# Kernel tuning notes

Measured on AMD Instinct MI355X. Metric: run time of the kernel, lower is better.

## Reference

```python
import jax, jax.numpy as jnp
import numpy as np

LRELU_SLOPE = 0.2
LN_EPS = 1e-5
BAND_EPS = 1e-8


def setup_inputs() -> dict:
    key = jax.random.key(0)
    ks = jax.random.split(key, 3)
    B, C, H, W = 32, 3, 1024, 1024
    num_bands, feat_dim = 16, 256
    fin = C * num_bands * 3  # 144
    x = jax.random.normal(ks[0], (B, C, H, W), dtype=jnp.float32)
    W1 = jax.random.normal(ks[1], (fin, feat_dim), dtype=jnp.float32) * 0.05
    b1 = jnp.zeros((feat_dim,), jnp.float32)
    W2 = jax.random.normal(ks[2], (feat_dim, feat_dim), dtype=jnp.float32) * 0.05
    b2 = jnp.zeros((feat_dim,), jnp.float32)
    gamma = jnp.ones((feat_dim,), jnp.float32)
    beta = jnp.zeros((feat_dim,), jnp.float32)
    return {"x": x, "W1": W1, "b1": b1, "W2": W2, "b2": b2, "gamma": gamma, "beta": beta}


def reference(x, W1, b1, W2, b2, gamma, beta):
    B, C, H, W = x.shape
    nb = W1.shape[0] // (C * 3)  # num_bands
    # --- FFT magnitude ---
    mag = jnp.abs(jnp.fft.rfft2(x, norm='ortho'))  # [B,C,H,Wr]
    Wr = mag.shape[-1]
    # --- radial bin index (exact same >= comparisons as the torch band loop) ---
    u = jnp.fft.rfftfreq(W).astype(mag.dtype)          # [Wr]
    v = jnp.fft.fftfreq(H).astype(mag.dtype)           # [H]
    radius = jnp.sqrt(u[None, :] ** 2 + v[:, None] ** 2)  # [H,Wr]
    max_r = radius.max()
    lowers = max_r * jnp.arange(nb + 1, dtype=mag.dtype) / nb  # i=0..nb
    # bin = (#thresholds <= radius) - 1 ; radius==max_r lands in segment nb (excluded)
    bins = jnp.sum(radius[..., None] >= lowers[None, None, :], axis=-1) - 1  # [H,Wr]
    seg = bins.reshape(-1).astype(jnp.int32)  # [H*Wr]
    K = nb + 1
    # --- single-pass segmented reductions over all pixels ---
    magf = mag.reshape(B * C, -1).T                      # [HWr, B*C]
    counts = jax.ops.segment_sum(jnp.ones(seg.shape, mag.dtype), seg, num_segments=K)  # [K]
    s1 = jax.ops.segment_sum(magf, seg, num_segments=K)             # [K, BC]
    s2 = jax.ops.segment_sum(magf * magf, seg, num_segments=K)      # [K, BC]
    mx = jax.ops.segment_max(magf, seg, num_segments=K)             # [K, BC]
    denom = counts[:, None] + BAND_EPS
    mean = s1 / denom
    # sum over band of (mag-mean)^2 = s2 - 2*mean*s1 + count*mean^2
    var = (s2 - 2.0 * mean * s1 + counts[:, None] * mean * mean) / denom
    # drop segment nb (radius == max_r is excluded by `radius < upper`), then sqrt
    mean = mean[:nb]
    var = jnp.maximum(var[:nb], 0.0)
    std = jnp.sqrt(var)
    # torch max is over mag*mask (zeros elsewhere) -> floor at 0
    mx = jnp.maximum(mx[:nb], 0.0)
    # --- assemble [B, nb*3*C] in band-major, (mean,max,std), channel order ---
    def to_bkc(a):
        return a.reshape(nb, B, C).transpose(1, 0, 2)  # [B, nb, C]
    feat_vec = jnp.stack([to_bkc(mean), to_bkc(mx), to_bkc(std)], axis=2)  # [B, nb, 3, C]
    feat_vec = feat_vec.reshape(B, nb * 3 * C)
    # --- MLP: Linear -> LeakyReLU(0.2) -> Linear -> LayerNorm ---
    h = feat_vec @ W1 + b1
    h = jnp.where(h >= 0, h, LRELU_SLOPE * h)
    h = h @ W2 + b2
    mu = jnp.mean(h, axis=-1, keepdims=True)
    va = jnp.mean((h - mu) ** 2, axis=-1, keepdims=True)
    return (h - mu) / jnp.sqrt(va + LN_EPS) * gamma + beta
```

## Files before the change

kernel.cpp:

```cpp
#include <hip/hip_runtime.h>
#include <hip/hip_fp16.h>
#include <math.h>

#define HH    1024
#define WWID  1024
#define WR    513
#define NIMG  96
#define NGRP  65
#define KSEG  17
#define FEAT  256
#define FIN   144

__device__ __forceinline__ float2 cmul(float2 a, float2 b) {
    return make_float2(a.x * b.x - a.y * b.y, a.x * b.y + a.y * b.x);
}

__device__ __forceinline__ int radial_bin(int hf, int k) {
    const float maxr = 0.707106781186547524f;
    float v = (float)(hf < 512 ? hf : hf - 1024) * (1.0f / 1024.0f);
    float u = (float)k * (1.0f / 1024.0f);
    float rad = sqrtf(u * u + v * v);
    int bin = 0;
#pragma unroll
    for (int l = 1; l <= 16; ++l) {
        float lower = (maxr * (float)l) * 0.0625f;
        bin += (rad >= lower) ? 1 : 0;
    }
    return bin;
}

__device__ __forceinline__ int fast_bin(float rad) {
    int c = (int)(rad * 22.62741699796952f);
    if (c > 16) c = 16;
    if (c < 16 && rad >= (0.707106781186547524f * (float)(c + 1)) * 0.0625f) c++;
    else if (rad < (0.707106781186547524f * (float)c) * 0.0625f) c--;
    return c;
}

__device__ __forceinline__ float2 wave_fft_AB(float2 a[16], int l) {
    constexpr float TW16C[8] = {1.f, 0.9238795325112867f, 0.7071067811865476f,
                                0.3826834323650898f, 0.f, -0.3826834323650898f,
                                -0.7071067811865476f, -0.9238795325112867f};
    constexpr float TW16S[8] = {0.f, -0.3826834323650898f, -0.7071067811865476f,
                                -0.9238795325112867f, -1.f, -0.9238795325112867f,
                                -0.7071067811865476f, -0.3826834323650898f};
#pragma unroll
    for (int m = 2; m <= 16; m <<= 1) {
        const int half = m >> 1;
        const int tstep = 16 / m;
#pragma unroll
        for (int bse = 0; bse < 16; bse += m) {
#pragma unroll
            for (int jj = 0; jj < 8; ++jj) {
                if (jj < half) {
                    float2 w = make_float2(TW16C[jj * tstep], TW16S[jj * tstep]);
                    float2 tv = cmul(a[bse + half + jj], w);
                    float2 u0 = a[bse + jj];
                    a[bse + jj]        = make_float2(u0.x + tv.x, u0.y + tv.y);
                    a[bse + half + jj] = make_float2(u0.x - tv.x, u0.y - tv.y);
                }
            }
        }
    }
    float ang = (float)l * (-6.28318530717958647692f / 1024.0f);
    float2 w1 = make_float2(__cosf(ang), __sinf(ang));
    float2 w2 = cmul(w1, w1);
    float2 w3 = cmul(w2, w1);
    float2 w4 = cmul(w2, w2);
    float2 w8 = cmul(w4, w4);
    float2 w12 = cmul(w8, w4);
    a[1] = cmul(a[1], w1);
    a[2] = cmul(a[2], w2);
    a[3] = cmul(a[3], w3);
#pragma unroll
    for (int r = 4; r < 16; ++r) {
        float2 hi = (r >> 2) == 1 ? w4 : ((r >> 2) == 2 ? w8 : w12);
        float2 p = cmul(a[r], hi);
        int lo = r & 3;
        if (lo == 1) p = cmul(p, w1);
        else if (lo == 2) p = cmul(p, w2);
        else if (lo == 3) p = cmul(p, w3);
        a[r] = p;
    }
    return cmul(w8, w8);
}

__device__ __forceinline__ void wave_fft_C(float2 a[16], int l, float2 u) {
#pragma unroll
    for (int half = 32; half >= 1; half >>= 1) {
        const bool up = (l & half) != 0;
        const float sgn = up ? -1.0f : 1.0f;
        const float twx = up ? -u.x : 1.0f;
        const float twy = up ? -u.y : 0.0f;
#pragma unroll
        for (int r = 0; r < 16; ++r) {
            float ox = __shfl_xor(a[r].x, half);
            float oy = __shfl_xor(a[r].y, half);
            float sx = fmaf(sgn, a[r].x, ox);
            float sy = fmaf(sgn, a[r].y, oy);
            a[r].x = fmaf(sx, twx, -(sy * twy));
            a[r].y = fmaf(sx, twy, sy * twx);
        }
        if (half > 1) u = cmul(u, u);
    }
}

static __device__ __constant__ int BR4[16] = {0,8,4,12,2,10,6,14,1,9,5,13,3,11,7,15};

__global__ __launch_bounds__(1024) void k_rowfft(const float* __restrict__ x,
                                                 __half2* __restrict__ interm,
                                                 int img0) {
    __shared__ __half2 tile[1024][17];
    const int t = threadIdx.x;
    const int w = t >> 6;
    const int l = t & 63;
    const int blk = blockIdx.x;
    const int iy = blockIdx.y;
    const int img = img0 + iy;
    const int hA = ((w & 7) << 6) + 2 * blk + (w >> 3);
    const int hB = hA + 512;

    const float* r1 = x + ((size_t)img * HH + hA) * WWID;
    const float* r2 = x + ((size_t)img * HH + hB) * WWID;
    float2 a[16];
#pragma unroll
    for (int j = 0; j < 16; ++j) {
        int i = l + 64 * j;
        a[BR4[j]] = make_float2(r1[i], r2[i]);
    }

    float2 u16 = wave_fft_AB(a, l);
    wave_fft_C(a, l, u16);

    const int b = (int)(__brev((unsigned)l) >> 26);
#pragma unroll
    for (int r = 0; r < 16; ++r) {
        int k = 16 * b + r;
        tile[k][w ^ (b & 15)] = __floats2half2_rn(a[r].x, a[r].y);
    }
    __syncthreads();

    __half2* gout = interm + (size_t)iy * 1024 * 512 + blk * 16;
#pragma unroll
    for (int it = 0; it < 16; ++it) {
        int idx = t + it * 1024;
        int k = idx >> 4;
        int s = idx & 15;
        gout[(size_t)k * 512 + s] = tile[k][s ^ ((k >> 4) & 15)];
    }
}

__global__ __launch_bounds__(512) void k_colfft(const __half2* __restrict__ interm,
                                                float* __restrict__ partials,
                                                int img0) {
    __shared__ float wsum[8][KSEG][2];
    __shared__ unsigned wmax[8][KSEG];
    const int t = threadIdx.x;
    const int g = blockIdx.x;
    const int iy = blockIdx.y;
    const int img = img0 + iy;
    const int wv = t >> 6;
    const int l = t & 63;
    const int k = g * 8 + wv;

    for (int i = t; i < 8 * KSEG; i += 512) {
        int w = i / KSEG, bb = i - w * KSEG;
        wsum[w][bb][0] = 0.f; wsum[w][bb][1] = 0.f; wmax[w][bb] = 0u;
    }
    __syncthreads();

    if (k <= 512) {
        const int kn = (1024 - k) & 1023;
        const uint4* ps = (const uint4*)(interm + ((size_t)iy * 1024 + k) * 512 + l * 8);
        const uint4* pn = (const uint4*)(interm + ((size_t)iy * 1024 + kn) * 512 + l * 8);
        union QU { uint4 q[2]; __half2 h[8]; } us, un;
        us.q[0] = ps[0]; us.q[1] = ps[1];
        un.q[0] = pn[0]; un.q[1] = pn[1];

        float2 a[16];
#pragma unroll
        for (int m = 0; m < 8; ++m) {
            float2 zs = __half22float2(us.h[m]);
            float2 zn = __half22float2(un.h[m]);
            a[BR4[m]]     = make_float2(0.5f * (zs.x + zn.x), 0.5f * (zs.y - zn.y));
            a[BR4[m + 8]] = make_float2(0.5f * (zs.y + zn.y), 0.5f * (zn.x - zs.x));
        }

        float2 u16 = wave_fft_AB(a, l);
        wave_fft_C(a, l, u16);

        const int b = (int)(__brev((unsigned)l) >> 26);
        const int h0 = 16 * b;
        const float uf = (float)k * (1.0f / 1024.0f);
        const float uu = uf * uf;
        float vf0 = (float)(h0 < 512 ? h0 : h0 - 1024) * (1.0f / 1024.0f);
        float vfF = (float)(h0 + 15 < 512 ? h0 + 15 : h0 + 15 - 1024) * (1.0f / 1024.0f);
        int binF = fast_bin(sqrtf(fmaf(vf0, vf0, uu)));
        int binL = fast_bin(sqrtf(fmaf(vfF, vfF, uu)));
        const int bHi = (binF > binL) ? binF : binL;
        const float Lmid = (0.707106781186547524f * (float)bHi) * 0.0625f;
        const float Lmid2 = Lmid * Lmid;

        float sA1 = 0.f, sA2 = 0.f, mA = 0.f;
        float sB1 = 0.f, sB2 = 0.f, mB = 0.f;
#pragma unroll
        for (int r = 0; r < 16; ++r) {
            int h = h0 + r;
            float vf = (float)(h < 512 ? h : h - 1024) * (1.0f / 1024.0f);
            float s = fmaf(vf, vf, uu);
            float2 z = a[r];
            float p2 = fmaf(z.x, z.x, z.y * z.y);
            float m = sqrtf(p2) * (1.0f / 1024.0f);
            float msq = p2 * (1.0f / 1048576.0f);
            bool c = (s >= Lmid2);
            sA1 += c ? m : 0.f;
            sA2 += c ? msq : 0.f;
            mA = fmaxf(mA, c ? m : 0.f);
            sB1 += c ? 0.f : m;
            sB2 += c ? 0.f : msq;
            mB = fmaxf(mB, c ? 0.f : m);
        }

        atomicAdd(&wsum[wv][bHi][0], sA1);
        atomicAdd(&wsum[wv][bHi][1], sA2);
        atomicMax(&wmax[wv][bHi], __float_as_uint(mA));
        if (bHi > 0) {
            atomicAdd(&wsum[wv][bHi - 1][0], sB1);
            atomicAdd(&wsum[wv][bHi - 1][1], sB2);
            atomicMax(&wmax[wv][bHi - 1], __float_as_uint(mB));
        }
    }
    __syncthreads();

    if (t < KSEG) {
        float aS = 0.f, bS = 0.f, cM = 0.f;
#pragma unroll
        for (int w = 0; w < 8; ++w) {
            aS += wsum[w][t][0];
            bS += wsum[w][t][1];
            cM = fmaxf(cM, __uint_as_float(wmax[w][t]));
        }
        float* dstp = partials + ((size_t)img * NGRP + g) * (KSEG * 3) + t * 3;
        dstp[0] = aS; dstp[1] = bS; dstp[2] = cM;
    }
}

__global__ __launch_bounds__(256) void k_counts(unsigned* __restrict__ counts) {
    int cnt[KSEG];
#pragma unroll
    for (int l = 0; l < KSEG; ++l) cnt[l] = 0;
    const int total = HH * WR;
    for (int idx = blockIdx.x * 256 + threadIdx.x; idx < total; idx += gridDim.x * 256) {
        int h = idx / WR;
        int k = idx - h * WR;
        int bin = radial_bin(h, k);
#pragma unroll
        for (int l = 0; l < KSEG; ++l) cnt[l] += (bin == l) ? 1 : 0;
    }
    const int lane = threadIdx.x & 63;
#pragma unroll
    for (int l = 0; l < KSEG; ++l) {
        int c = cnt[l];
        for (int off = 32; off > 0; off >>= 1) c += __shfl_xor(c, off);
        if (lane == 0 && c > 0) atomicAdd(&counts[l], (unsigned)c);
    }
}

__global__ __launch_bounds__(256) void k_mlp(const float* __restrict__ partials,
                                             const unsigned* __restrict__ counts,
                                             const float* __restrict__ W1,
                                             const float* __restrict__ b1,
                                             const float* __restrict__ W2,
                                             const float* __restrict__ b2,
                                             const float* __restrict__ gamma,
                                             const float* __restrict__ beta,
                                             float* __restrict__ out) {
    __shared__ float feat[FIN];
    __shared__ float h1s[FEAT];
    __shared__ float red[FEAT];
    const int b = blockIdx.x;
    const int t = threadIdx.x;
    if (t < 48) {
        int c = t / 16;
        int bin = t % 16;
        const float* p = partials + ((size_t)(b * 3 + c) * NGRP) * (KSEG * 3) + bin * 3;
        float s1 = 0.f, s2 = 0.f, mxv = 0.f;
        for (int gg = 0; gg < NGRP; ++gg) {
            s1 += p[gg * (KSEG * 3) + 0];
            s2 += p[gg * (KSEG * 3) + 1];
            mxv = fmaxf(mxv, p[gg * (KSEG * 3) + 2]);
        }
        float cntf = (float)counts[bin];
        float denom = cntf + 1e-8f;
        float mean = s1 / denom;
        float var = (s2 - 2.0f * mean * s1 + cntf * mean * mean) / denom;
        var = fmaxf(var, 0.0f);
        float sd = sqrtf(var);
        mxv = fmaxf(mxv, 0.0f);
        feat[bin * 9 + 0 + c] = mean;
        feat[bin * 9 + 3 + c] = mxv;
        feat[bin * 9 + 6 + c] = sd;
    }
    __syncthreads();

    float acc = b1[t];
    for (int i = 0; i < FIN; ++i) acc += feat[i] * W1[i * FEAT + t];
    acc = (acc >= 0.0f) ? acc : 0.2f * acc;
    h1s[t] = acc;
    __syncthreads();

    float acc2 = b2[t];
    for (int i = 0; i < FEAT; ++i) acc2 += h1s[i] * W2[i * FEAT + t];

    red[t] = acc2;
    __syncthreads();
    for (int off = 128; off > 0; off >>= 1) {
        if (t < off) red[t] += red[t + off];
        __syncthreads();
    }
    float mu = red[0] * (1.0f / 256.0f);
    __syncthreads();
    float dvt = acc2 - mu;
    red[t] = dvt * dvt;
    __syncthreads();
    for (int off = 128; off > 0; off >>= 1) {
        if (t < off) red[t] += red[t + off];
        __syncthreads();
    }
    float va = red[0] * (1.0f / 256.0f);
    out[(size_t)b * FEAT + t] = dvt / sqrtf(va + 1e-5f) * gamma[t] + beta[t];
}

extern "C" void kernel_launch(void* const* d_in, const int* in_sizes, int n_in,
                              void* d_out, int out_size, void* d_ws, size_t ws_size,
                              hipStream_t stream) {
    const float* x     = (const float*)d_in[0];
    const float* W1    = (const float*)d_in[1];
    const float* b1    = (const float*)d_in[2];
    const float* W2    = (const float*)d_in[3];
    const float* b2    = (const float*)d_in[4];
    const float* gamma = (const float*)d_in[5];
    const float* beta  = (const float*)d_in[6];
    float* out = (float*)d_out;

    char* ws = (char*)d_ws;
    unsigned* counts = (unsigned*)ws;
    float* partials = (float*)(ws + 256);
    const size_t partialsBytes = (size_t)NIMG * NGRP * KSEG * 3 * sizeof(float);
    const size_t intermOff = (256 + partialsBytes + 255) & ~(size_t)255;
    __half2* interm = (__half2*)(ws + intermOff);
    const size_t perImg = (size_t)1024 * 512 * sizeof(__half2);

    long long avail = (long long)ws_size - (long long)intermOff;
    int chunk = (avail > 0) ? (int)(avail / (long long)perImg) : 0;
    if (chunk > NIMG) chunk = NIMG;
    if (chunk < 1) chunk = 1;

    hipMemsetAsync(counts, 0, KSEG * sizeof(unsigned), stream);
    k_counts<<<dim3(128), dim3(256), 0, stream>>>(counts);

    for (int img0 = 0; img0 < NIMG; img0 += chunk) {
        int n = NIMG - img0;
        if (n > chunk) n = chunk;
        k_rowfft<<<dim3(32, n), dim3(1024), 0, stream>>>(x, interm, img0);
        k_colfft<<<dim3(NGRP, n), dim3(512), 0, stream>>>(interm, partials, img0);
    }

    k_mlp<<<dim3(32), dim3(256), 0, stream>>>(partials, counts, W1, b1, W2, b2,
                                              gamma, beta, out);
}
```

Before: 447.0 us.

## Restructure row FFT for vectorized loads, swizzle shuffles, and slotted LDS atomics

The row FFT now loads each row with contiguous float4 reads and reverses the decomposition order: the cross-lane stages run first, then twiddles, then the in-register radix-16. This lets each lane hold contiguous input elements. Cross-lane shuffles use ds_swizzle for lane distances below 32 and ds_bpermute for 32, replacing generic shfl_xor. In the column kernel, the shared-memory atomic accumulators are spread over 8 slots per wave to cut contention, and the 1/1024 scaling is moved out of the inner loop. The risks are a larger shared-memory footprint, a duplicated init loop, and the removed XOR swizzle on the row tile, which may bring back LDS bank conflicts.

```diff
diff --git a/kernel.cpp b/kernel.cpp
--- a/kernel.cpp
+++ b/kernel.cpp
@@ -37,7 +37,45 @@
     return c;
 }
 
-__device__ __forceinline__ float2 wave_fft_AB(float2 a[16], int l) {
+__device__ constexpr int BR4[16] = {0,8,4,12,2,10,6,14,1,9,5,13,3,11,7,15};
+
+template<int HALF>
+__device__ __forceinline__ float sxl(float v, int addr32) {
+    if constexpr (HALF == 32)
+        return __int_as_float(__builtin_amdgcn_ds_bpermute(addr32, __float_as_int(v)));
+    else
+        return __int_as_float(__builtin_amdgcn_ds_swizzle(__float_as_int(v),
+                                                          (HALF << 10) | 0x1F));
+}
+
+template<int HALF>
+__device__ __forceinline__ void fftC_stage(float2 a[16], int l, float2 u, int addr32) {
+    const bool up = (l & HALF) != 0;
+    const float sgn = up ? -1.0f : 1.0f;
+    const float twx = up ? -u.x : 1.0f;
+    const float twy = up ? -u.y : 0.0f;
+#pragma unroll
+    for (int r = 0; r < 16; ++r) {
+        float ox = sxl<HALF>(a[r].x, addr32);
+        float oy = sxl<HALF>(a[r].y, addr32);
+        float sx = fmaf(sgn, a[r].x, ox);
+        float sy = fmaf(sgn, a[r].y, oy);
+        a[r].x = fmaf(sx, twx, -(sy * twy));
+        a[r].y = fmaf(sx, twy, sy * twx);
+    }
+}
+
+__device__ __forceinline__ void wave_fft_C(float2 a[16], int l, float2 u) {
+    const int addr32 = ((l ^ 32) << 2);
+    fftC_stage<32>(a, l, u, addr32); u = cmul(u, u);
+    fftC_stage<16>(a, l, u, addr32); u = cmul(u, u);
+    fftC_stage<8>(a, l, u, addr32);  u = cmul(u, u);
+    fftC_stage<4>(a, l, u, addr32);  u = cmul(u, u);
+    fftC_stage<2>(a, l, u, addr32);  u = cmul(u, u);
+    fftC_stage<1>(a, l, u, addr32);
+}
+
+__device__ __forceinline__ void fft16_regs(float2 a[16]) {
     constexpr float TW16C[8] = {1.f, 0.9238795325112867f, 0.7071067811865476f,
                                 0.3826834323650898f, 0.f, -0.3826834323650898f,
                                 -0.7071067811865476f, -0.9238795325112867f};
@@ -62,50 +100,31 @@
             }
         }
     }
-    float ang = (float)l * (-6.28318530717958647692f / 1024.0f);
+}
+
+template<bool PERM>
+__device__ __forceinline__ void twiddle_regs(float2 a[16], float ang, float2* w16out) {
     float2 w1 = make_float2(__cosf(ang), __sinf(ang));
     float2 w2 = cmul(w1, w1);
     float2 w3 = cmul(w2, w1);
     float2 w4 = cmul(w2, w2);
     float2 w8 = cmul(w4, w4);
     float2 w12 = cmul(w8, w4);
-    a[1] = cmul(a[1], w1);
-    a[2] = cmul(a[2], w2);
-    a[3] = cmul(a[3], w3);
-#pragma unroll
-    for (int r = 4; r < 16; ++r) {
-        float2 hi = (r >> 2) == 1 ? w4 : ((r >> 2) == 2 ? w8 : w12);
-        float2 p = cmul(a[r], hi);
-        int lo = r & 3;
+#pragma unroll
+    for (int r = 1; r < 16; ++r) {
+        const int e = PERM ? BR4[r] : r;
+        float2 p = a[r];
+        const int hi = e >> 2, lo = e & 3;
+        if (hi == 1) p = cmul(p, w4);
+        else if (hi == 2) p = cmul(p, w8);
+        else if (hi == 3) p = cmul(p, w12);
         if (lo == 1) p = cmul(p, w1);
         else if (lo == 2) p = cmul(p, w2);
         else if (lo == 3) p = cmul(p, w3);
         a[r] = p;
     }
-    return cmul(w8, w8);
-}
-
-__device__ __forceinline__ void wave_fft_C(float2 a[16], int l, float2 u) {
-#pragma unroll
-    for (int half = 32; half >= 1; half >>= 1) {
-        const bool up = (l & half) != 0;
-        const float sgn = up ? -1.0f : 1.0f;
-        const float twx = up ? -u.x : 1.0f;
-        const float twy = up ? -u.y : 0.0f;
-#pragma unroll
-        for (int r = 0; r < 16; ++r) {
-            float ox = __shfl_xor(a[r].x, half);
-            float oy = __shfl_xor(a[r].y, half);
-            float sx = fmaf(sgn, a[r].x, ox);
-            float sy = fmaf(sgn, a[r].y, oy);
-            a[r].x = fmaf(sx, twx, -(sy * twy));
-            a[r].y = fmaf(sx, twy, sy * twx);
-        }
-        if (half > 1) u = cmul(u, u);
-    }
-}
-
-static __device__ __constant__ int BR4[16] = {0,8,4,12,2,10,6,14,1,9,5,13,3,11,7,15};
+    if (w16out) *w16out = cmul(w8, w8);
+}
 
 __global__ __launch_bounds__(1024) void k_rowfft(const float* __restrict__ x,
                                                  __half2* __restrict__ interm,
@@ -120,24 +139,33 @@
     const int hA = ((w & 7) << 6) + 2 * blk + (w >> 3);
     const int hB = hA + 512;
 
-    const float* r1 = x + ((size_t)img * HH + hA) * WWID;
-    const float* r2 = x + ((size_t)img * HH + hB) * WWID;
+    const float4* r1 = (const float4*)(x + ((size_t)img * HH + hA) * WWID) + 4 * l;
+    const float4* r2 = (const float4*)(x + ((size_t)img * HH + hB) * WWID) + 4 * l;
+    float4 f1[4], f2[4];
+#pragma unroll
+    for (int c = 0; c < 4; ++c) { f1[c] = r1[c]; f2[c] = r2[c]; }
+
     float2 a[16];
 #pragma unroll
     for (int j = 0; j < 16; ++j) {
-        int i = l + 64 * j;
-        a[BR4[j]] = make_float2(r1[i], r2[i]);
-    }
-
-    float2 u16 = wave_fft_AB(a, l);
-    wave_fft_C(a, l, u16);
+        float v1 = ((const float*)f1)[j];
+        float v2 = ((const float*)f2)[j];
+        a[BR4[j]] = make_float2(v1, v2);
+    }
+
+    float angL = (float)l * (-6.28318530717958647692f / 64.0f);
+    wave_fft_C(a, l, make_float2(__cosf(angL), __sinf(angL)));
 
     const int b = (int)(__brev((unsigned)l) >> 26);
-#pragma unroll
-    for (int r = 0; r < 16; ++r) {
-        int k = 16 * b + r;
-        tile[k][w ^ (b & 15)] = __floats2half2_rn(a[r].x, a[r].y);
-    }
+
+    float angB = (float)b * (-6.28318530717958647692f / 1024.0f);
+    twiddle_regs<true>(a, angB, nullptr);
+
+    fft16_regs(a);
+
+#pragma unroll
+    for (int r = 0; r < 16; ++r)
+        tile[b + 64 * r][w] = __floats2half2_rn(a[r].x, a[r].y);
     __syncthreads();
 
     __half2* gout = interm + (size_t)iy * 1024 * 512 + blk * 16;
@@ -146,15 +174,15 @@
         int idx = t + it * 1024;
         int k = idx >> 4;
         int s = idx & 15;
-        gout[(size_t)k * 512 + s] = tile[k][s ^ ((k >> 4) & 15)];
+        gout[(size_t)k * 512 + s] = tile[k][s];
     }
 }
 
 __global__ __launch_bounds__(512) void k_colfft(const __half2* __restrict__ interm,
                                                 float* __restrict__ partials,
                                                 int img0) {
-    __shared__ float wsum[8][KSEG][2];
-    __shared__ unsigned wmax[8][KSEG];
+    __shared__ float wsum[8][KSEG][8][2];
+    __shared__ unsigned wmax[8][KSEG][8];
     const int t = threadIdx.x;
     const int g = blockIdx.x;
     const int iy = blockIdx.y;
@@ -162,10 +190,25 @@
     const int wv = t >> 6;
     const int l = t & 63;
     const int k = g * 8 + wv;
-
-    for (int i = t; i < 8 * KSEG; i += 512) {
-        int w = i / KSEG, bb = i - w * KSEG;
-        wsum[w][bb][0] = 0.f; wsum[w][bb][1] = 0.f; wmax[w][bb] = 0u;
+    const int slot = l & 7;
+
+    for (int i = t; i < 8 * KSEG * 8; i += 512) {
+        int w = i >> 7;
+        int rem = i - w * 136;
+        if (w < 8 && rem < 136) {
+            int bb = rem >> 3, sl = rem & 7;
+            wsum[w][bb][sl][0] = 0.f;
+            wsum[w][bb][sl][1] = 0.f;
+            wmax[w][bb][sl] = 0u;
+        }
+    }
+    for (int i = t; i < 8 * 136; i += 512) {
+        int w = i / 136;
+        int rem = i - w * 136;
+        int bb = rem >> 3, sl = rem & 7;
+        wsum[w][bb][sl][0] = 0.f;
+        wsum[w][bb][sl][1] = 0.f;
+        wmax[w][bb][sl] = 0u;
     }
     __syncthreads();
 
@@ -186,15 +229,19 @@
             a[BR4[m + 8]] = make_float2(0.5f * (zs.y + zn.y), 0.5f * (zn.x - zs.x));
         }
 
-        float2 u16 = wave_fft_AB(a, l);
+        fft16_regs(a);
+        float2 u16;
+        float angB = (float)l * (-6.28318530717958647692f / 1024.0f);
+        twiddle_regs<false>(a, angB, &u16);
         wave_fft_C(a, l, u16);
 
         const int b = (int)(__brev((unsigned)l) >> 26);
         const int h0 = 16 * b;
+        const float vbase = (float)(h0 < 512 ? h0 : h0 - 1024);
         const float uf = (float)k * (1.0f / 1024.0f);
         const float uu = uf * uf;
-        float vf0 = (float)(h0 < 512 ? h0 : h0 - 1024) * (1.0f / 1024.0f);
-        float vfF = (float)(h0 + 15 < 512 ? h0 + 15 : h0 + 15 - 1024) * (1.0f / 1024.0f);
+        float vf0 = vbase * (1.0f / 1024.0f);
+        float vfF = (vbase + 15.0f) * (1.0f / 1024.0f);
         int binF = fast_bin(sqrtf(fmaf(vf0, vf0, uu)));
         int binL = fast_bin(sqrtf(fmaf(vfF, vfF, uu)));
         const int bHi = (binF > binL) ? binF : binL;
@@ -205,29 +252,29 @@
         float sB1 = 0.f, sB2 = 0.f, mB = 0.f;
 #pragma unroll
         for (int r = 0; r < 16; ++r) {
-            int h = h0 + r;
-            float vf = (float)(h < 512 ? h : h - 1024) * (1.0f / 1024.0f);
+            float vf = (vbase + (float)r) * (1.0f / 1024.0f);
             float s = fmaf(vf, vf, uu);
             float2 z = a[r];
             float p2 = fmaf(z.x, z.x, z.y * z.y);
-            float m = sqrtf(p2) * (1.0f / 1024.0f);
-            float msq = p2 * (1.0f / 1048576.0f);
+            float m = sqrtf(p2);
             bool c = (s >= Lmid2);
             sA1 += c ? m : 0.f;
-            sA2 += c ? msq : 0.f;
+            sA2 += c ? p2 : 0.f;
             mA = fmaxf(mA, c ? m : 0.f);
             sB1 += c ? 0.f : m;
-            sB2 += c ? 0.f : msq;
+            sB2 += c ? 0.f : p2;
             mB = fmaxf(mB, c ? 0.f : m);
         }
-
-        atomicAdd(&wsum[wv][bHi][0], sA1);
-        atomicAdd(&wsum[wv][bHi][1], sA2);
-        atomicMax(&wmax[wv][bHi], __float_as_uint(mA));
+        const float c1 = 1.0f / 1024.0f;
+        const float c2 = 1.0f / 1048576.0f;
+
+        atomicAdd(&wsum[wv][bHi][slot][0], sA1 * c1);
+        atomicAdd(&wsum[wv][bHi][slot][1], sA2 * c2);
+        atomicMax(&wmax[wv][bHi][slot], __float_as_uint(mA * c1));
         if (bHi > 0) {
-            atomicAdd(&wsum[wv][bHi - 1][0], sB1);
-            atomicAdd(&wsum[wv][bHi - 1][1], sB2);
-            atomicMax(&wmax[wv][bHi - 1], __float_as_uint(mB));
+            atomicAdd(&wsum[wv][bHi - 1][slot][0], sB1 * c1);
+            atomicAdd(&wsum[wv][bHi - 1][slot][1], sB2 * c2);
+            atomicMax(&wmax[wv][bHi - 1][slot], __float_as_uint(mB * c1));
         }
     }
     __syncthreads();
@@ -235,11 +282,13 @@
     if (t < KSEG) {
         float aS = 0.f, bS = 0.f, cM = 0.f;
 #pragma unroll
-        for (int w = 0; w < 8; ++w) {
-            aS += wsum[w][t][0];
-            bS += wsum[w][t][1];
-            cM = fmaxf(cM, __uint_as_float(wmax[w][t]));
-        }
+        for (int w = 0; w < 8; ++w)
+#pragma unroll
+            for (int sl = 0; sl < 8; ++sl) {
+                aS += wsum[w][t][sl][0];
+                bS += wsum[w][t][sl][1];
+                cM = fmaxf(cM, __uint_as_float(wmax[w][t][sl]));
+            }
         float* dstp = partials + ((size_t)img * NGRP + g) * (KSEG * 3) + t * 3;
         dstp[0] = aS; dstp[1] = bS; dstp[2] = cM;
     }
```

Result: faster. 432.1 us (-3.3%).
